# Kernel tuning notes

Measured on AMD Instinct MI355X. Metric: run time of the kernel, lower is better.

Reference implementation:

```python
import jax, jax.numpy as jnp
import numpy as np


def conv2d(x, w, b):
    # x: [B, Cin, H, W], w: [Cout, Cin, 3, 3] -> SAME 3x3 conv, stride 1
    y = jax.lax.conv_general_dilated(x, w, (1, 1), 'SAME',
                                     dimension_numbers=('NCHW', 'OIHW', 'NCHW'))
    return y + b[None, :, None, None]


def trilinear_interpolation(data, offsets, sample_nums):
    """data: [B, D(frames), C, H, W]; offsets: [B, sample_nums*3, H, W]
    Returns samples [B, sample_nums, C, H, W] via trilinear interp over (d,h,w)."""
    B, D, C, H, W = data.shape
    S = sample_nums
    off = offsets.reshape(B, S, 3, H, W)
    # base 3x3x3 grid centered at middle frame / current pixel
    g = jnp.arange(S)
    kd = (g // 9 - 1).astype(jnp.float32)        # [S]
    kh = ((g // 3) % 3 - 1).astype(jnp.float32)
    kw = (g % 3 - 1).astype(jnp.float32)
    center = (D - 1) / 2.0
    hh = jnp.arange(H, dtype=jnp.float32)
    ww = jnp.arange(W, dtype=jnp.float32)
    pd = center + kd[None, :, None, None] + off[:, :, 0]                 # [B,S,H,W]
    ph = hh[None, None, :, None] + kh[None, :, None, None] + off[:, :, 1]
    pw = ww[None, None, None, :] + kw[None, :, None, None] + off[:, :, 2]
    pd = jnp.clip(pd, 0.0, D - 1.0)
    ph = jnp.clip(ph, 0.0, H - 1.0)
    pw = jnp.clip(pw, 0.0, W - 1.0)
    d0 = jnp.floor(pd); h0 = jnp.floor(ph); w0 = jnp.floor(pw)
    fd = pd - d0; fh = ph - h0; fw = pw - w0
    d0i = d0.astype(jnp.int32); h0i = h0.astype(jnp.int32); w0i = w0.astype(jnp.int32)
    d1i = jnp.minimum(d0i + 1, D - 1)
    h1i = jnp.minimum(h0i + 1, H - 1)
    w1i = jnp.minimum(w0i + 1, W - 1)
    # flatten (d,h,w) for gather, keep channels contiguous
    data_flat = data.transpose(0, 2, 1, 3, 4).reshape(B, C, D * H * W)

    def gather(di, hi, wi):
        idx = ((di * H + hi) * W + wi).reshape(B, 1, S * H * W)
        g_ = jnp.take_along_axis(data_flat, idx, axis=2)   # [B,C,S*H*W]
        return g_.reshape(B, C, S, H, W).transpose(0, 2, 1, 3, 4)  # [B,S,C,H,W]

    out = jnp.zeros((B, S, C, H, W), dtype=data.dtype)
    for di, wd in ((d0i, 1.0 - fd), (d1i, fd)):
        for hi, wh in ((h0i, 1.0 - fh), (h1i, fh)):
            for wi, wwgt in ((w0i, 1.0 - fw), (w1i, fw)):
                wgt = (wd * wh * wwgt)[:, :, None]  # [B,S,1,H,W]
                out = out + wgt * gather(di, hi, wi)
    return out


SAMPLE_NUMS = 27
GROUPS = 3


def setup_inputs() -> dict:
    key = jax.random.key(0)
    ks = jax.random.split(key, 14)
    B, BURST, C, H, W = 4, 5, 3, 256, 256
    in_len = BURST * C          # 15
    ch_w = in_len + 128 + SAMPLE_NUMS * C  # 224
    s = 0.05
    p = lambda k, sh: jax.random.normal(k, sh, dtype=jnp.float32) * s
    return {
        'data': jax.random.normal(ks[0], (B, BURST, C, H, W), dtype=jnp.float32),
        'enc_w1': p(ks[1], (64, in_len, 3, 3)), 'enc_b1': jnp.zeros((64,), jnp.float32),
        'enc_w2': p(ks[2], (128, 64, 3, 3)),    'enc_b2': jnp.zeros((128,), jnp.float32),
        'off_w':  p(ks[3], (SAMPLE_NUMS * 3, 128, 3, 3)), 'off_b': jnp.zeros((SAMPLE_NUMS * 3,), jnp.float32),
        'wc_w1':  p(ks[4], (64, ch_w, 3, 3)),   'wc_b1': jnp.zeros((64,), jnp.float32),
        'wc_w2':  p(ks[5], (64, 64, 3, 3)),     'wc_b2': jnp.zeros((64,), jnp.float32),
        'wc_w3':  p(ks[6], (SAMPLE_NUMS, 64, 3, 3)), 'wc_b3': jnp.zeros((SAMPLE_NUMS,), jnp.float32),
    }


def reference(data, enc_w1, enc_b1, enc_w2, enc_b2, off_w, off_b,
              wc_w1, wc_b1, wc_w2, wc_b2, wc_w3, wc_b3):
    B, D, C, H, W = data.shape
    net_feed = data.reshape(B, D * C, H, W)
    # encoder_decoder proxy: feature [B,128,H,W] + offsets [B,81,H,W]
    f1 = jax.nn.relu(conv2d(net_feed, enc_w1, enc_b1))
    feature = jax.nn.relu(conv2d(f1, enc_w2, enc_b2))
    offsets = conv2d(feature, off_w, off_b)
    samples = trilinear_interpolation(data, offsets, SAMPLE_NUMS)  # [B,S,C,H,W]
    weight_feed = jnp.concatenate([net_feed, feature,
                                   samples.reshape(B, SAMPLE_NUMS * C, H, W)], axis=1)
    h1 = jax.nn.relu(conv2d(weight_feed, wc_w1, wc_b1))
    h2 = jax.nn.relu(conv2d(h1, wc_w2, wc_b2))
    weights = conv2d(h2, wc_w3, wc_b3)  # [B,S,H,W]
    cpg = SAMPLE_NUMS // GROUPS
    s_g = samples.reshape(B, GROUPS, cpg, C, H, W)
    w_g = weights.reshape(B, GROUPS, cpg, H, W)
    # per-group weighted kernel-prediction sum (convolution_3D), scaled by g
    res_i = GROUPS * jnp.einsum('bgkchw,bgkhw->bgchw', s_g, w_g)
    out = jnp.sum(res_i, axis=1) / GROUPS
    return res_i, out, samples
```

## Files before the change

kernel.cpp:

```cpp
#include <hip/hip_runtime.h>


typedef __attribute__((ext_vector_type(8))) short short8;
typedef __attribute__((ext_vector_type(4))) float f32x4;

__device__ __forceinline__ unsigned short f2bf(float f) {
    unsigned int b = __float_as_uint(f);
    b = (b + 0x7fffu + ((b >> 16) & 1u)) >> 16;
    return (unsigned short)b;
}
__device__ __forceinline__ float bf2f(unsigned int u) {
    return __uint_as_float(u << 16);
}
__device__ __forceinline__ unsigned int pack2(float a, float b) {
    return (unsigned int)f2bf(a) | ((unsigned int)f2bf(b) << 16);
}

__global__ __launch_bounds__(256) void prep_kern(
    const float* __restrict__ w1, const float* __restrict__ w2,
    const float* __restrict__ w3, const float* __restrict__ w5,
    const float* __restrict__ w6, const float* __restrict__ w7,
    unsigned short* __restrict__ wpk)
{
    int idx = blockIdx.x * 256 + threadIdx.x;
    if (idx < 460800) {
        const float* w; int off, CinR, CoutR, CoutP, nch, remap;
        if (idx < 18432)       { w = w1; off = 0;      CinR = 15;  CoutR = 64;  CoutP = 64;  nch = 1; remap = 0; }
        else if (idx < 92160)  { w = w2; off = 18432;  CinR = 64;  CoutR = 128; CoutP = 128; nch = 2; remap = 0; }
        else if (idx < 239616) { w = w3; off = 92160;  CinR = 128; CoutR = 81;  CoutP = 128; nch = 4; remap = 0; }
        else if (idx < 387072) { w = w5; off = 239616; CinR = 224; CoutR = 64;  CoutP = 64;  nch = 8; remap = 1; }
        else if (idx < 423936) { w = w6; off = 387072; CinR = 64;  CoutR = 64;  CoutP = 64;  nch = 2; remap = 0; }
        else                   { w = w7; off = 423936; CinR = 64;  CoutR = 27;  CoutP = 64;  nch = 2; remap = 0; }
        int li = idx - off;
        int kin = li & 31;
        int t = li >> 5;
        int co = t % CoutP; t /= CoutP;
        int chunk = t % nch;
        int tap = t / nch;
        int ci = chunk * 32 + kin;
        int cs = -1;
        if (remap) {
            if (ci < 15) cs = ci;
            else if (ci >= 16 && ci <= 224) cs = ci - 1;
        } else {
            if (ci < CinR) cs = ci;
        }
        float val = 0.f;
        if (co < CoutR && cs >= 0)
            val = w[(co * CinR + cs) * 9 + tap];
        wpk[idx] = f2bf(val);
    } else if (idx < 460800 + 8192) {
        wpk[idx] = 0;
    }
}

__global__ __launch_bounds__(256) void convert_data(
    const float* __restrict__ data, unsigned short* __restrict__ concat)
{
    int i = blockIdx.x * 256 + threadIdx.x;
    int b = i >> 16, p = i & 65535;
    int base = i * 232;
#pragma unroll
    for (int c = 0; c < 15; ++c)
        concat[base + c] = f2bf(data[(b * 15 + c) * 65536 + p]);
    concat[base + 15] = 0;
}

__global__ __launch_bounds__(256) void conv_mfma(
    const unsigned short* __restrict__ src, int srcCs, int srcOff,
    const unsigned short* __restrict__ wp, const float* __restrict__ bias,
    int nch, int Cout, int Cout_pad,
    void* __restrict__ dst, int dstCs, int dstOff, int mode, int relu,
    const uint4* __restrict__ zp)
{
    __shared__ uint4 ldsb[2][1584];
    const int tid = threadIdx.x;
    const int lane = tid & 63;
    const int wv = tid >> 6;
    const int bx = blockIdx.x, b = blockIdx.y, bz = blockIdx.z;
    const int x0 = (bx & 3) * 64, y0 = (bx >> 2) * 4;
    const int l15 = lane & 15, l4 = lane >> 4;
    const int mtc = min(4, (Cout - bz * 64 + 15) >> 4);

    f32x4 acc[4][4];
#pragma unroll
    for (int m = 0; m < 4; ++m)
#pragma unroll
        for (int nt = 0; nt < 4; ++nt) acc[m][nt] = (f32x4)0.f;

    auto stage = [&](int buf, int chunk) {
        int ch = srcOff + chunk * 32 + wv * 8;
        bool chok = (ch + 8 <= srcCs);
        const unsigned short* sbase = src + ch;
#pragma unroll
        for (int it = 0; it < 7; ++it) {
            int r = it * 64 + lane;
            if (r < 396) {
                int hy = r / 66, hx = r - hy * 66;
                int y = y0 - 1 + hy, x = x0 - 1 + hx;
                const uint4* g;
                if (chok && (unsigned)y < 256u && (unsigned)x < 256u)
                    g = (const uint4*)(sbase + (b * 65536 + y * 256 + x) * srcCs);
                else
                    g = zp + lane;
                __builtin_amdgcn_global_load_lds(
                    (const __attribute__((address_space(1))) void*)g,
                    (__attribute__((address_space(3))) void*)&ldsb[buf][wv * 396 + it * 64],
                    16, 0, 0);
            }
        }
    };

    stage(0, 0);
    int buf = 0;
    for (int c = 0; c < nch; ++c) {
        __syncthreads();
        if (c + 1 < nch) stage(buf ^ 1, c + 1);
#pragma unroll
        for (int tap = 0; tap < 9; ++tap) {
            const int dy = tap / 3, dx = tap - dy * 3;
            short8 af[4];
#pragma unroll
            for (int m = 0; m < 4; ++m)
                if (m < mtc)
                    af[m] = *(const short8*)(wp +
                        ((tap * nch + c) * Cout_pad + bz * 64 + m * 16 + l15) * 32 + l4 * 8);
#pragma unroll
            for (int nt = 0; nt < 4; ++nt) {
                int hx = nt * 16 + l15 + dx;
                int hy = wv + dy;
                short8 bf = __builtin_bit_cast(short8,
                    ldsb[buf][l4 * 396 + hy * 66 + hx]);
#pragma unroll
                for (int m = 0; m < 4; ++m)
                    if (m < mtc)
                        acc[m][nt] = __builtin_amdgcn_mfma_f32_16x16x32_bf16(
                            af[m], bf, acc[m][nt], 0, 0, 0);
            }
        }
        buf ^= 1;
    }

    const int y = y0 + wv;
#pragma unroll
    for (int m = 0; m < 4; ++m) {
        if (m >= mtc) continue;
        int co0 = bz * 64 + m * 16 + l4 * 4;
#pragma unroll
        for (int nt = 0; nt < 4; ++nt) {
            int x = x0 + nt * 16 + l15;
            float v[4];
#pragma unroll
            for (int e = 0; e < 4; ++e) {
                int co = co0 + e;
                float f = acc[m][nt][e] + ((co < Cout) ? bias[co] : 0.f);
                if (relu) f = fmaxf(f, 0.f);
                v[e] = f;
            }
            if (mode == 0) {
                unsigned short* d = (unsigned short*)dst +
                    ((b * 65536 + y * 256 + x) * dstCs + dstOff + co0);
                if (co0 + 3 < Cout) {
                    uint2 pk = make_uint2(pack2(v[0], v[1]), pack2(v[2], v[3]));
                    *(uint2*)d = pk;
                } else {
#pragma unroll
                    for (int e = 0; e < 4; ++e)
                        if (co0 + e < Cout) d[e] = f2bf(v[e]);
                }
            } else {
                float* d = (float*)dst + (b * dstCs + co0) * 65536 + y * 256 + x;
#pragma unroll
                for (int e = 0; e < 4; ++e)
                    if (co0 + e < Cout) d[e * 65536] = v[e];
            }
        }
    }
}

__global__ __launch_bounds__(256) void trilin_kern(
    const float* __restrict__ data, unsigned short* __restrict__ concat,
    float* __restrict__ smp)
{
    int i = blockIdx.x * 256 + threadIdx.x;
    int b = i >> 16, p = i & 65535;
    int y = p >> 8, x = p & 255;
    unsigned short* cptr = concat + i * 232 + 144;

    unsigned int wbuf[41];
    {
        const uint4* gp = (const uint4*)cptr;
#pragma unroll
        for (int k = 0; k < 10; ++k) {
            uint4 t = gp[k];
            wbuf[4 * k] = t.x; wbuf[4 * k + 1] = t.y;
            wbuf[4 * k + 2] = t.z; wbuf[4 * k + 3] = t.w;
        }
        wbuf[40] = (unsigned int)cptr[80];
    }

#pragma unroll
    for (int s = 0; s < 27; ++s) {
        int L0 = 3 * s;
        float o0 = bf2f((wbuf[L0 >> 1] >> ((L0 & 1) * 16)) & 0xffffu);
        float o1 = bf2f((wbuf[(L0 + 1) >> 1] >> (((L0 + 1) & 1) * 16)) & 0xffffu);
        float o2 = bf2f((wbuf[(L0 + 2) >> 1] >> (((L0 + 2) & 1) * 16)) & 0xffffu);

        float kd = (float)(s / 9 - 1);
        float kh = (float)((s / 3) % 3 - 1);
        float kw = (float)(s % 3 - 1);
        float pd = 2.0f + kd + o0;
        float ph = (float)y + kh + o1;
        float pw = (float)x + kw + o2;
        pd = fminf(fmaxf(pd, 0.f), 4.f);
        ph = fminf(fmaxf(ph, 0.f), 255.f);
        pw = fminf(fmaxf(pw, 0.f), 255.f);
        float d0 = floorf(pd), h0 = floorf(ph), w0 = floorf(pw);
        float fd = pd - d0, fh = ph - h0, fw = pw - w0;
        int d0i = (int)d0, h0i = (int)h0, w0i = (int)w0;
        int d1i = min(d0i + 1, 4), h1i = min(h0i + 1, 255), w1i = min(w0i + 1, 255);

        float res[3];
#pragma unroll
        for (int c = 0; c < 3; ++c) {
            const float* dp = data + ((b * 5 + d0i) * 3 + c) * 65536;
            const float* dp1 = data + ((b * 5 + d1i) * 3 + c) * 65536;
            int a00 = (h0i << 8) + w0i, a01 = (h0i << 8) + w1i;
            int a10 = (h1i << 8) + w0i, a11 = (h1i << 8) + w1i;
            float r0 = (dp[a00] * (1.f - fw) + dp[a01] * fw) * (1.f - fh)
                     + (dp[a10] * (1.f - fw) + dp[a11] * fw) * fh;
            float r1 = (dp1[a00] * (1.f - fw) + dp1[a01] * fw) * (1.f - fh)
                     + (dp1[a10] * (1.f - fw) + dp1[a11] * fw) * fh;
            float r = r0 * (1.f - fd) + r1 * fd;
            res[c] = r;
            smp[((b * 27 + s) * 3 + c) * 65536 + p] = r;
        }
#pragma unroll
        for (int c = 0; c < 3; ++c) {
            int L = L0 + c;
            unsigned int u = (unsigned int)f2bf(res[c]);
            if (L & 1) wbuf[L >> 1] = (wbuf[L >> 1] & 0xffffu) | (u << 16);
            else       wbuf[L >> 1] = (wbuf[L >> 1] & 0xffff0000u) | u;
        }
    }

    wbuf[40] &= 0xffffu;
    uint4* gp = (uint4*)cptr;
#pragma unroll
    for (int k = 0; k < 10; ++k)
        gp[k] = make_uint4(wbuf[4 * k], wbuf[4 * k + 1], wbuf[4 * k + 2], wbuf[4 * k + 3]);
    *(unsigned int*)(cptr + 80) = wbuf[40];
}

__global__ __launch_bounds__(256) void combine_kern(
    const float* __restrict__ smp, const float* __restrict__ wt,
    float* __restrict__ res_i, float* __restrict__ outp)
{
    int i = blockIdx.x * 256 + threadIdx.x;
    int p = i & 65535;
    int b = i >> 16;
    float ov[3] = {0.f, 0.f, 0.f};
#pragma unroll
    for (int g = 0; g < 3; ++g) {
        float r[3] = {0.f, 0.f, 0.f};
#pragma unroll
        for (int k = 0; k < 9; ++k) {
            int s = g * 9 + k;
            float w = wt[((b * 27 + s) << 16) + p];
#pragma unroll
            for (int c = 0; c < 3; ++c)
                r[c] = fmaf(smp[(((b * 27 + s) * 3 + c) << 16) + p], w, r[c]);
        }
#pragma unroll
        for (int c = 0; c < 3; ++c) {
            res_i[(((b * 3 + g) * 3 + c) << 16) + p] = 3.f * r[c];
            ov[c] += r[c];
        }
    }
#pragma unroll
    for (int c = 0; c < 3; ++c)
        outp[((b * 3 + c) << 16) + p] = ov[c];
}

extern "C" void kernel_launch(void* const* d_in, const int* in_sizes, int n_in,
                              void* d_out, int out_size, void* d_ws, size_t ws_size,
                              hipStream_t stream)
{
    const float* data   = (const float*)d_in[0];
    const float* enc_w1 = (const float*)d_in[1];
    const float* enc_b1 = (const float*)d_in[2];
    const float* enc_w2 = (const float*)d_in[3];
    const float* enc_b2 = (const float*)d_in[4];
    const float* off_w  = (const float*)d_in[5];
    const float* off_b  = (const float*)d_in[6];
    const float* wc_w1  = (const float*)d_in[7];
    const float* wc_b1  = (const float*)d_in[8];
    const float* wc_w2  = (const float*)d_in[9];
    const float* wc_b2  = (const float*)d_in[10];
    const float* wc_w3  = (const float*)d_in[11];
    const float* wc_b3  = (const float*)d_in[12];

    float* dout  = (float*)d_out;
    float* res_i = dout;
    float* outp  = dout + 2359296;
    float* smp   = dout + 3145728;

    char* ws = (char*)d_ws;
    unsigned short* concat = (unsigned short*)ws;
    unsigned short* buf_a  = (unsigned short*)(ws + 121634816);
    unsigned short* buf_b  = (unsigned short*)(ws + 155189248);
    unsigned short* wpk    = (unsigned short*)(ws + 188743680);
    unsigned short* wp1 = wpk;
    unsigned short* wp2 = wpk + 18432;
    unsigned short* wp3 = wpk + 92160;
    unsigned short* wp5 = wpk + 239616;
    unsigned short* wp6 = wpk + 387072;
    unsigned short* wp7 = wpk + 423936;
    const uint4* zp = (const uint4*)(wpk + 460800);
    float* wconv = (float*)buf_a;

    dim3 blk(256);

    prep_kern<<<1832, blk, 0, stream>>>(enc_w1, enc_w2, off_w, wc_w1, wc_w2, wc_w3, wpk);
    convert_data<<<1024, blk, 0, stream>>>(data, concat);

    conv_mfma<<<dim3(256, 4, 1), blk, 0, stream>>>(
        concat, 232, 0, wp1, enc_b1, 1, 64, 64, buf_a, 64, 0, 0, 1, zp);
    conv_mfma<<<dim3(256, 4, 2), blk, 0, stream>>>(
        buf_a, 64, 0, wp2, enc_b2, 2, 128, 128, concat, 232, 16, 0, 1, zp);
    conv_mfma<<<dim3(256, 4, 2), blk, 0, stream>>>(
        concat, 232, 16, wp3, off_b, 4, 81, 128, concat, 232, 144, 0, 0, zp);
    trilin_kern<<<1024, blk, 0, stream>>>(data, concat, smp);
    conv_mfma<<<dim3(256, 4, 1), blk, 0, stream>>>(
        concat, 232, 0, wp5, wc_b1, 8, 64, 64, buf_a, 64, 0, 0, 1, zp);
    conv_mfma<<<dim3(256, 4, 1), blk, 0, stream>>>(
        buf_a, 64, 0, wp6, wc_b2, 2, 64, 64, buf_b, 64, 0, 0, 1, zp);
    conv_mfma<<<dim3(256, 4, 1), blk, 0, stream>>>(
        buf_b, 64, 0, wp7, wc_b3, 2, 27, 64, wconv, 27, 0, 1, 0, zp);
    combine_kern<<<1024, blk, 0, stream>>>(smp, wconv, res_i, outp);
}
```

Measured before the change: 814.5 us.

## Fuse final conv with combine and gather trilinear taps from packed bf16 data

```diff
diff --git a/kernel.cpp b/kernel.cpp
--- a/kernel.cpp
+++ b/kernel.cpp
@@ -66,6 +66,17 @@
     concat[base + 15] = 0;
 }
 
+__global__ __launch_bounds__(256) void pack_dpk(
+    const float* __restrict__ data, unsigned short* __restrict__ dpk)
+{
+    int i = blockIdx.x * 256 + threadIdx.x;
+    int bd = i >> 16, p = i & 65535;
+    unsigned int w0 = pack2(data[(bd * 3 + 0) * 65536 + p],
+                            data[(bd * 3 + 1) * 65536 + p]);
+    unsigned int w1 = (unsigned int)f2bf(data[(bd * 3 + 2) * 65536 + p]);
+    *(uint2*)(dpk + i * 4) = make_uint2(w0, w1);
+}
+
 __global__ __launch_bounds__(256) void conv_mfma(
     const unsigned short* __restrict__ src, int srcCs, int srcOff,
     const unsigned short* __restrict__ wp, const float* __restrict__ bias,
@@ -178,8 +189,142 @@
     }
 }
 
+__global__ __launch_bounds__(256) void conv7_combine(
+    const unsigned short* __restrict__ src,
+    const unsigned short* __restrict__ wp,
+    const float* __restrict__ bias,
+    const unsigned short* __restrict__ concat,
+    float* __restrict__ res_i, float* __restrict__ outp,
+    const uint4* __restrict__ zp)
+{
+    __shared__ char ldsraw[50688];
+    uint4 (*ldsb)[1584] = (uint4(*)[1584])ldsraw;
+    float* wlds = (float*)ldsraw;
+    const int tid = threadIdx.x;
+    const int lane = tid & 63;
+    const int wv = tid >> 6;
+    const int bx = blockIdx.x, b = blockIdx.y;
+    const int x0 = (bx & 3) * 64, y0 = (bx >> 2) * 4;
+    const int l15 = lane & 15, l4 = lane >> 4;
+
+    f32x4 acc[2][4];
+#pragma unroll
+    for (int m = 0; m < 2; ++m)
+#pragma unroll
+        for (int nt = 0; nt < 4; ++nt) acc[m][nt] = (f32x4)0.f;
+
+    auto stage = [&](int buf, int chunk) {
+        int ch = chunk * 32 + wv * 8;
+        const unsigned short* sbase = src + ch;
+#pragma unroll
+        for (int it = 0; it < 7; ++it) {
+            int r = it * 64 + lane;
+            if (r < 396) {
+                int hy = r / 66, hx = r - hy * 66;
+                int y = y0 - 1 + hy, x = x0 - 1 + hx;
+                const uint4* g;
+                if ((unsigned)y < 256u && (unsigned)x < 256u)
+                    g = (const uint4*)(sbase + (b * 65536 + y * 256 + x) * 64);
+                else
+                    g = zp + lane;
+                __builtin_amdgcn_global_load_lds(
+                    (const __attribute__((address_space(1))) void*)g,
+                    (__attribute__((address_space(3))) void*)&ldsb[buf][wv * 396 + it * 64],
+                    16, 0, 0);
+            }
+        }
+    };
+
+    stage(0, 0);
+    int buf = 0;
+    for (int c = 0; c < 2; ++c) {
+        __syncthreads();
+        if (c + 1 < 2) stage(buf ^ 1, c + 1);
+#pragma unroll
+        for (int tap = 0; tap < 9; ++tap) {
+            const int dy = tap / 3, dx = tap - dy * 3;
+            short8 af[2];
+#pragma unroll
+            for (int m = 0; m < 2; ++m)
+                af[m] = *(const short8*)(wp +
+                    ((tap * 2 + c) * 64 + m * 16 + l15) * 32 + l4 * 8);
+#pragma unroll
+            for (int nt = 0; nt < 4; ++nt) {
+                int hx = nt * 16 + l15 + dx;
+                int hy = wv + dy;
+                short8 bf = __builtin_bit_cast(short8,
+                    ldsb[buf][l4 * 396 + hy * 66 + hx]);
+#pragma unroll
+                for (int m = 0; m < 2; ++m)
+                    acc[m][nt] = __builtin_amdgcn_mfma_f32_16x16x32_bf16(
+                        af[m], bf, acc[m][nt], 0, 0, 0);
+            }
+        }
+        buf ^= 1;
+    }
+
+    __syncthreads();
+#pragma unroll
+    for (int m = 0; m < 2; ++m) {
+        int co0 = m * 16 + l4 * 4;
+#pragma unroll
+        for (int nt = 0; nt < 4; ++nt) {
+            int px = nt * 16 + l15;
+#pragma unroll
+            for (int e = 0; e < 4; ++e) {
+                int co = co0 + e;
+                wlds[wv * 2112 + px * 33 + co] =
+                    acc[m][nt][e] + ((co < 27) ? bias[co] : 0.f);
+            }
+        }
+    }
+    __syncthreads();
+
+    const int r = tid >> 6, px = tid & 63;
+    const float* wl = wlds + r * 2112 + px * 33;
+    const int y = y0 + r, x = x0 + px;
+    const int p = y * 256 + x;
+    const unsigned short* cp = concat + (b * 65536 + p) * 232 + 144;
+    unsigned int sw[41];
+    {
+        const uint4* gp = (const uint4*)cp;
+#pragma unroll
+        for (int k = 0; k < 10; ++k) {
+            uint4 t = gp[k];
+            sw[4 * k] = t.x; sw[4 * k + 1] = t.y;
+            sw[4 * k + 2] = t.z; sw[4 * k + 3] = t.w;
+        }
+        sw[40] = (unsigned int)cp[80];
+    }
+    float ov[3] = {0.f, 0.f, 0.f};
+#pragma unroll
+    for (int g = 0; g < 3; ++g) {
+        float rr[3] = {0.f, 0.f, 0.f};
+#pragma unroll
+        for (int k = 0; k < 9; ++k) {
+            int s = g * 9 + k;
+            float w = wl[s];
+            int L0 = 3 * s;
+            float s0 = bf2f((sw[L0 >> 1] >> ((L0 & 1) * 16)) & 0xffffu);
+            float s1 = bf2f((sw[(L0 + 1) >> 1] >> (((L0 + 1) & 1) * 16)) & 0xffffu);
+            float s2 = bf2f((sw[(L0 + 2) >> 1] >> (((L0 + 2) & 1) * 16)) & 0xffffu);
+            rr[0] = fmaf(s0, w, rr[0]);
+            rr[1] = fmaf(s1, w, rr[1]);
+            rr[2] = fmaf(s2, w, rr[2]);
+        }
+#pragma unroll
+        for (int c = 0; c < 3; ++c) {
+            res_i[(b * 9 + g * 3 + c) * 65536 + p] = 3.f * rr[c];
+            ov[c] += rr[c];
+        }
+    }
+#pragma unroll
+    for (int c = 0; c < 3; ++c)
+        outp[(b * 3 + c) * 65536 + p] = ov[c];
+}
+
 __global__ __launch_bounds__(256) void trilin_kern(
-    const float* __restrict__ data, unsigned short* __restrict__ concat,
+    const unsigned short* __restrict__ dpk, unsigned short* __restrict__ concat,
     float* __restrict__ smp)
 {
     int i = blockIdx.x * 256 + threadIdx.x;
@@ -220,17 +365,27 @@
         int d0i = (int)d0, h0i = (int)h0, w0i = (int)w0;
         int d1i = min(d0i + 1, 4), h1i = min(h0i + 1, 255), w1i = min(w0i + 1, 255);
 
+        const unsigned short* p0 = dpk + (b * 5 + d0i) * 262144;
+        const unsigned short* p1 = dpk + (b * 5 + d1i) * 262144;
+        int a00 = ((h0i << 8) + w0i) << 2, a01 = ((h0i << 8) + w1i) << 2;
+        int a10 = ((h1i << 8) + w0i) << 2, a11 = ((h1i << 8) + w1i) << 2;
+        uint2 q000 = *(const uint2*)(p0 + a00), q001 = *(const uint2*)(p0 + a01);
+        uint2 q010 = *(const uint2*)(p0 + a10), q011 = *(const uint2*)(p0 + a11);
+        uint2 q100 = *(const uint2*)(p1 + a00), q101 = *(const uint2*)(p1 + a01);
+        uint2 q110 = *(const uint2*)(p1 + a10), q111 = *(const uint2*)(p1 + a11);
+
         float res[3];
 #pragma unroll
         for (int c = 0; c < 3; ++c) {
-            const float* dp = data + ((b * 5 + d0i) * 3 + c) * 65536;
-            const float* dp1 = data + ((b * 5 + d1i) * 3 + c) * 65536;
-            int a00 = (h0i << 8) + w0i, a01 = (h0i << 8) + w1i;
-            int a10 = (h1i << 8) + w0i, a11 = (h1i << 8) + w1i;
-            float r0 = (dp[a00] * (1.f - fw) + dp[a01] * fw) * (1.f - fh)
-                     + (dp[a10] * (1.f - fw) + dp[a11] * fw) * fh;
-            float r1 = (dp1[a00] * (1.f - fw) + dp1[a01] * fw) * (1.f - fh)
-                     + (dp1[a10] * (1.f - fw) + dp1[a11] * fw) * fh;
+            auto ex = [&](uint2 q) {
+                unsigned int u = (c == 0) ? (q.x & 0xffffu)
+                              : (c == 1) ? (q.x >> 16) : (q.y & 0xffffu);
+                return bf2f(u);
+            };
+            float r0 = (ex(q000) * (1.f - fw) + ex(q001) * fw) * (1.f - fh)
+                     + (ex(q010) * (1.f - fw) + ex(q011) * fw) * fh;
+            float r1 = (ex(q100) * (1.f - fw) + ex(q101) * fw) * (1.f - fh)
+                     + (ex(q110) * (1.f - fw) + ex(q111) * fw) * fh;
             float r = r0 * (1.f - fd) + r1 * fd;
             res[c] = r;
             smp[((b * 27 + s) * 3 + c) * 65536 + p] = r;
@@ -250,36 +405,6 @@
     for (int k = 0; k < 10; ++k)
         gp[k] = make_uint4(wbuf[4 * k], wbuf[4 * k + 1], wbuf[4 * k + 2], wbuf[4 * k + 3]);
     *(unsigned int*)(cptr + 80) = wbuf[40];
-}
-
-__global__ __launch_bounds__(256) void combine_kern(
-    const float* __restrict__ smp, const float* __restrict__ wt,
-    float* __restrict__ res_i, float* __restrict__ outp)
-{
-    int i = blockIdx.x * 256 + threadIdx.x;
-    int p = i & 65535;
-    int b = i >> 16;
-    float ov[3] = {0.f, 0.f, 0.f};
-#pragma unroll
-    for (int g = 0; g < 3; ++g) {
-        float r[3] = {0.f, 0.f, 0.f};
-#pragma unroll
-        for (int k = 0; k < 9; ++k) {
-            int s = g * 9 + k;
-            float w = wt[((b * 27 + s) << 16) + p];
-#pragma unroll
-            for (int c = 0; c < 3; ++c)
-                r[c] = fmaf(smp[(((b * 27 + s) * 3 + c) << 16) + p], w, r[c]);
-        }
-#pragma unroll
-        for (int c = 0; c < 3; ++c) {
-            res_i[(((b * 3 + g) * 3 + c) << 16) + p] = 3.f * r[c];
-            ov[c] += r[c];
-        }
-    }
-#pragma unroll
-    for (int c = 0; c < 3; ++c)
-        outp[((b * 3 + c) << 16) + p] = ov[c];
 }
 
 extern "C" void kernel_launch(void* const* d_in, const int* in_sizes, int n_in,
@@ -317,12 +442,13 @@
     unsigned short* wp6 = wpk + 387072;
     unsigned short* wp7 = wpk + 423936;
     const uint4* zp = (const uint4*)(wpk + 460800);
-    float* wconv = (float*)buf_a;
+    unsigned short* dpk = buf_b;
 
     dim3 blk(256);
 
     prep_kern<<<1832, blk, 0, stream>>>(enc_w1, enc_w2, off_w, wc_w1, wc_w2, wc_w3, wpk);
     convert_data<<<1024, blk, 0, stream>>>(data, concat);
+    pack_dpk<<<5120, blk, 0, stream>>>(data, dpk);
 
     conv_mfma<<<dim3(256, 4, 1), blk, 0, stream>>>(
         concat, 232, 0, wp1, enc_b1, 1, 64, 64, buf_a, 64, 0, 0, 1, zp);
@@ -330,12 +456,11 @@
         buf_a, 64, 0, wp2, enc_b2, 2, 128, 128, concat, 232, 16, 0, 1, zp);
     conv_mfma<<<dim3(256, 4, 2), blk, 0, stream>>>(
         concat, 232, 16, wp3, off_b, 4, 81, 128, concat, 232, 144, 0, 0, zp);
-    trilin_kern<<<1024, blk, 0, stream>>>(data, concat, smp);
+    trilin_kern<<<1024, blk, 0, stream>>>(dpk, concat, smp);
     conv_mfma<<<dim3(256, 4, 1), blk, 0, stream>>>(
         concat, 232, 0, wp5, wc_b1, 8, 64, 64, buf_a, 64, 0, 0, 1, zp);
     conv_mfma<<<dim3(256, 4, 1), blk, 0, stream>>>(
         buf_a, 64, 0, wp6, wc_b2, 2, 64, 64, buf_b, 64, 0, 0, 1, zp);
-    conv_mfma<<<dim3(256, 4, 1), blk, 0, stream>>>(
-        buf_b, 64, 0, wp7, wc_b3, 2, 27, 64, wconv, 27, 0, 1, 0, zp);
-    combine_kern<<<1024, blk, 0, stream>>>(smp, wconv, res_i, outp);
-}
+    conv7_combine<<<dim3(256, 4), blk, 0, stream>>>(
+        buf_b, wp7, wc_b3, concat, res_i, outp, zp);
+}
```

Result: faster. 744.2 us (-8.6%).
